# Optimization experiments

Measured on AMD Instinct MI355X. Metric: run time of the kernel, lower is better.

## Reference

```python
import jax, jax.numpy as jnp
import numpy as np

N, T, F = 4096, 24, 16          # nodes, seq_len, in_features
H = 128                          # temporal_hidden
NH, DO = 4, 32                   # gat num_heads, gat out_features (NH*DO == H)
SEM, PH = 64, 32                 # semantic hidden, predictor hidden
SLOPE = 0.2                      # leaky_relu negative slope
ADJ_P = 0.01                     # adjacency density


def setup_inputs() -> dict:
    key = jax.random.key(0)
    ks = jax.random.split(key, 40)
    f32 = jnp.float32

    def rn(k, shape, s=0.02):
        return jax.random.normal(k, shape, f32) * s

    features = jax.random.normal(ks[0], (N, T, F), f32)
    pos_adj = (jax.random.uniform(ks[1], (N, N)) < ADJ_P).astype(f32)
    neg_adj = (jax.random.uniform(ks[2], (N, N)) < ADJ_P).astype(f32)

    inp = dict(features=features, pos_adj=pos_adj, neg_adj=neg_adj)
    # GRU (torch layout: W_ih [3H,F], W_hh [3H,H], gate order r,z,n)
    inp['gru_Wih'] = rn(ks[3], (3 * H, F), 1.0 / np.sqrt(H))
    inp['gru_Whh'] = rn(ks[4], (3 * H, H), 1.0 / np.sqrt(H))
    inp['gru_bih'] = rn(ks[5], (3 * H,), 1.0 / np.sqrt(H))
    inp['gru_bhh'] = rn(ks[6], (3 * H,), 1.0 / np.sqrt(H))
    # GAT params (linear weights stored [in, out] so we use x @ W)
    i = 7
    for pre in ('pos', 'neg'):
        inp[pre + '_W'] = rn(ks[i], (H, NH * DO)); i += 1
        inp[pre + '_u'] = rn(ks[i], (NH, DO, 1), 1.0); i += 1
        inp[pre + '_v'] = rn(ks[i], (NH, DO, 1), 1.0); i += 1
        inp[pre + '_b'] = rn(ks[i], (1, NH * DO)); i += 1
        inp[pre + '_pW'] = rn(ks[i], (H, NH * DO)); i += 1
        inp[pre + '_pb'] = jnp.zeros((NH * DO,), f32)
    inp['self_W'] = rn(ks[i], (H, H)); i += 1
    inp['self_b'] = jnp.zeros((H,), f32)
    inp['mpos_W'] = rn(ks[i], (NH * DO, H)); i += 1
    inp['mpos_b'] = jnp.zeros((H,), f32)
    inp['mneg_W'] = rn(ks[i], (NH * DO, H)); i += 1
    inp['mneg_b'] = jnp.zeros((H,), f32)
    inp['sem_W1'] = rn(ks[i], (H, SEM)); i += 1
    inp['sem_b1'] = jnp.zeros((SEM,), f32)
    inp['sem_W2'] = rn(ks[i], (SEM, 1)); i += 1
    inp['pred_W1'] = rn(ks[i], (H, PH)); i += 1
    inp['pred_b1'] = jnp.zeros((PH,), f32)
    inp['pred_W2'] = rn(ks[i], (PH, 1)); i += 1
    inp['pred_b2'] = jnp.zeros((1,), f32)
    return inp


def _gru_last(x, Wih, Whh, bih, bhh):
    # x: [N, T, F] -> last hidden state [N, H]
    gi_all = jnp.einsum('ntf,gf->tng', x, Wih) + bih  # precompute input gates [T,N,3H]
    h0 = jnp.zeros((x.shape[0], Whh.shape[1]), x.dtype)

    def step(h, gi):
        gh = h @ Whh.T + bhh
        ir, iz, in_ = jnp.split(gi, 3, axis=-1)
        hr, hz, hn = jnp.split(gh, 3, axis=-1)
        r = jax.nn.sigmoid(ir + hr)
        z = jax.nn.sigmoid(iz + hz)
        n = jnp.tanh(in_ + r * hn)
        return (1.0 - z) * n + z * h, None

    h, _ = jax.lax.scan(step, h0, gi_all)
    return h


def _gat(x, adj, W, u, v, b, pW, pb):
    sup = (x @ W).reshape(-1, NH, DO).transpose(1, 0, 2)     # [NH, N, DO]
    f1 = jnp.matmul(sup, u).reshape(NH, 1, -1)               # [NH, 1, N]
    f2 = jnp.matmul(sup, v).reshape(NH, -1, 1)               # [NH, N, 1]
    w = jax.nn.leaky_relu(f1 + f2, SLOPE)                    # [NH, N, N]
    mw = w * adj                                             # mask
    rs = mw.sum(axis=2, keepdims=True)
    rs = jnp.where(rs == 0, jnp.ones_like(rs), rs)
    attn = mw / rs
    out = jnp.matmul(attn, sup).transpose(1, 0, 2).reshape(-1, NH * DO)
    return out + b + x @ pW + pb                             # bias + residual


def _pairnorm_si(x):
    x = x - x.mean(axis=0)
    rn = jnp.sqrt(1e-6 + (x * x).sum(axis=1, keepdims=True))
    return x / rn


def reference(features, pos_adj, neg_adj,
              gru_Wih, gru_Whh, gru_bih, gru_bhh,
              pos_W, pos_u, pos_v, pos_b, pos_pW, pos_pb,
              neg_W, neg_u, neg_v, neg_b, neg_pW, neg_pb,
              self_W, self_b, mpos_W, mpos_b, mneg_W, mneg_b,
              sem_W1, sem_b1, sem_W2,
              pred_W1, pred_b1, pred_W2, pred_b2):
    support = _gru_last(features, gru_Wih, gru_Whh, gru_bih, gru_bhh)  # [N, H]
    pos_sup = _gat(support, pos_adj, pos_W, pos_u, pos_v, pos_b, pos_pW, pos_pb)
    neg_sup = _gat(support, neg_adj, neg_W, neg_u, neg_v, neg_b, neg_pW, neg_pb)
    self_e = support @ self_W + self_b
    pos_e = pos_sup @ mpos_W + mpos_b
    neg_e = neg_sup @ mneg_W + mneg_b
    emb = jnp.stack([self_e, pos_e, neg_e], axis=1)          # [N, 3, H]
    w = jnp.tanh(emb @ sem_W1 + sem_b1) @ sem_W2             # [N, 3, 1]
    beta = jax.nn.softmax(w, axis=1)
    fused = (beta * emb).sum(axis=1)                          # [N, H]
    fused = _pairnorm_si(fused)
    h = jax.nn.relu(fused @ pred_W1 + pred_b1)               # dropout is eval no-op
    out = jax.nn.sigmoid(h @ pred_W2 + pred_b2).squeeze(-1)  # [N]
    return out
```

## Files before the change

### kernel.cpp

```cpp
#include <hip/hip_runtime.h>


#define NN 4096

typedef unsigned short u16;
typedef unsigned int   u32;
typedef unsigned long long u64;
typedef __attribute__((ext_vector_type(8))) short  short8;
typedef __attribute__((ext_vector_type(4))) float  float4v;

__device__ inline float bf2f(u16 u){ return __uint_as_float(((u32)u)<<16); }
__device__ inline u16 f2bf(float f){
  u32 x = __float_as_uint(f);
  return (u16)((x + 0x7fffu + ((x>>16)&1u))>>16);
}
__device__ inline float ldm(const void* p, int i, int bf){
  return bf ? bf2f(((const u16*)p)[i]) : ((const float*)p)[i];
}
__device__ inline u16 ldm16(const void* p, int i, int bf){
  return bf ? ((const u16*)p)[i] : f2bf(((const float*)p)[i]);
}
__device__ inline float fexp(float x){
  x = fminf(fmaxf(x,-80.f),80.f);
  return __builtin_amdgcn_exp2f(x*1.4426950408889634f);
}
__device__ inline float sigm_fast(float x){
  return __builtin_amdgcn_rcpf(1.f + __builtin_amdgcn_exp2f(-x*1.4426950408889634f));
}
__device__ inline float tanhf_(float x){
  float c = fminf(fmaxf(x,-15.f),15.f);
  float e = __builtin_amdgcn_exp2f(c*2.8853900817779268f);
  return (e-1.f)*__builtin_amdgcn_rcpf(e+1.f);
}
__device__ inline float4v mfma16(short8 a, short8 b, float4v c){
  return __builtin_amdgcn_mfma_f32_16x16x32_bf16(a,b,c,0,0,0);
}
__device__ inline int rdbf(const int* __restrict__ mflag){
  int b=0;
  #pragma unroll
  for (int k=0;k<16;k++) b|=mflag[k];
  return b;
}

__global__ __launch_bounds__(256) void k_detect(const u32* __restrict__ adj,
                                                int* __restrict__ mflag)
{
  __shared__ u32 w4[4];
  const int lane=threadIdx.x&63, wv=threadIdx.x>>6;
  int i = (blockIdx.x*256 + threadIdx.x)*4;
  uint4 v = *(const uint4*)(adj + i);
  u32 acc = (v.x | v.y | v.z | v.w) & 0xFFFFu;
  unsigned long long b = __ballot(acc != 0);
  if (lane==0) w4[wv] = (b!=0);
  __syncthreads();
  if (threadIdx.x==0) mflag[blockIdx.x] = (w4[0]|w4[1]|w4[2]|w4[3]) ? 1 : 0;
}

__global__ __launch_bounds__(256) void k_imp(
  const int* __restrict__ mflag,
  const void* gWih, const void* gWhh, const void* gbih, const void* gbhh,
  const void* posW, const void* posu, const void* posv, const void* posb,
  const void* pospW, const void* pospb,
  const void* negW, const void* negu, const void* negv, const void* negb,
  const void* negpW, const void* negpb,
  const void* selfW, const void* selfb, const void* mposW, const void* mposb,
  const void* mnegW, const void* mnegb,
  const void* semW1, const void* semb1, const void* semW2,
  const void* predW1, const void* predb1, const void* predW2, const void* predb2,
  u16* __restrict__ Wihb, u16* __restrict__ Whhb,
  u16* __restrict__ WT1,  u16* __restrict__ WT2,
  float* __restrict__ cbrz, float* __restrict__ cbin, float* __restrict__ cbhn,
  float* __restrict__ cuv,  float* __restrict__ cgb,  float* __restrict__ csb,
  float* __restrict__ cw1t, float* __restrict__ cb1,  float* __restrict__ cw2,
  float* __restrict__ cpw1t, float* __restrict__ cpb1, float* __restrict__ cpw2,
  float* __restrict__ cpb2, float* __restrict__ meanacc)
{
  const int bf = rdbf(mflag);
  int i = blockIdx.x*256 + threadIdx.x;
  if (i < 6144){ Wihb[i]=ldm16(gWih,i,bf); return; }  i-=6144;
  if (i < 49152){ Whhb[i]=ldm16(gWhh,i,bf); return; } i-=49152;
  if (i < 81920){
    int m=i>>7,k=i&127,sel=m>>7,ml=m&127;
    const void* s = sel==0?posW: sel==1?pospW: sel==2?negW: sel==3?negpW: selfW;
    WT1[i]=ldm16(s,k*128+ml,bf); return;
  } i-=81920;
  if (i < 32768){
    int m=i>>7,k=i&127;
    const void* s = (m<128)? mposW : mnegW;
    WT2[i]=ldm16(s,k*128+(m&127),bf); return;
  } i-=32768;
  if (i < 256){ cbrz[i]=ldm(gbih,i,bf)+ldm(gbhh,i,bf); return; } i-=256;
  if (i < 128){ cbin[i]=ldm(gbih,256+i,bf); return; } i-=128;
  if (i < 128){ cbhn[i]=ldm(gbhh,256+i,bf); return; } i-=128;
  if (i < 512){
    int s=i>>8, rem=i&255, wh=rem>>7, hd=rem&127;
    const void* p = s? (wh? negv:negu) : (wh? posv:posu);
    cuv[i]=ldm(p,hd,bf); return;
  } i-=512;
  if (i < 256){
    int s=i>>7, d=i&127;
    cgb[i]=ldm(s?negb:posb,d,bf)+ldm(s?negpb:pospb,d,bf); return;
  } i-=256;
  if (i < 384){
    int t=i>>7, d=i&127;
    const void* p = t==0? selfb : t==1? mposb : mnegb;
    csb[i]=ldm(p,d,bf); return;
  } i-=384;
  if (i < 8448){
    int c=i/132, k=i-c*132;
    cw1t[i] = (k<128)? ldm(semW1,k*64+c,bf) : 0.f; return;
  } i-=8448;
  if (i < 64){ cb1[i]=ldm(semb1,i,bf); return; } i-=64;
  if (i < 64){ cw2[i]=ldm(semW2,i,bf); return; } i-=64;
  if (i < 4224){
    int c=i/132, k=i-c*132;
    cpw1t[i] = (k<128)? ldm(predW1,k*32+c,bf) : 0.f; return;
  } i-=4224;
  if (i < 32){ cpb1[i]=ldm(predb1,i,bf); return; } i-=32;
  if (i < 32){ cpw2[i]=ldm(predW2,i,bf); return; } i-=32;
  if (i < 1){ cpb2[i]=ldm(predb2,i,bf); return; } i-=1;
  if (i < 128){ meanacc[i]=0.f; return; }
}

__global__ __launch_bounds__(512) void k_gruf(
  const int* __restrict__ mflag, const void* feat,
  const u16* __restrict__ Wihb, const u16* __restrict__ Whhb,
  const float* __restrict__ cbrz, const float* __restrict__ cbin,
  const float* __restrict__ cbhn,
  const u16* __restrict__ WT1, const float* __restrict__ cuv,
  const void* posadj, const void* negadj,
  u16* __restrict__ csri, int* __restrict__ csrc,
  u16* __restrict__ C1b, float* __restrict__ f12)
{
  __shared__ __attribute__((aligned(16))) u16 sh_x[16*392];
  __shared__ __attribute__((aligned(16))) u16 hbuf[2][16*136];
  const int bf = rdbf(mflag);
  const int tid=threadIdx.x, lane=tid&63, wv=tid>>6;

  if (blockIdx.x >= NN/16){
    const int c = blockIdx.x - NN/16;
    const int s = c >> 9;
    const int i = (c & 511)*8 + wv;
    const void* adj = s? negadj : posadj;
    u64 mask=0;
    if (bf){
      const u16* rp = (const u16*)adj + (size_t)i*4096;
      #pragma unroll
      for (int it=0; it<8; it++){
        const uint4 vv = *(const uint4*)(rp + it*512 + lane*8);
        u32 w[4]={vv.x,vv.y,vv.z,vv.w};
        #pragma unroll
        for (int q=0;q<4;q++){
          if (w[q]&0xffffu) mask |= 1ull<<(it*8+2*q);
          if (w[q]>>16)     mask |= 1ull<<(it*8+2*q+1);
        }
      }
    } else {
      const float* rp = (const float*)adj + (size_t)i*4096;
      #pragma unroll
      for (int it=0; it<16; it++){
        const uint4 vv = *(const uint4*)(rp + it*256 + lane*4);
        if (vv.x) mask |= 1ull<<(it*4+0);
        if (vv.y) mask |= 1ull<<(it*4+1);
        if (vv.z) mask |= 1ull<<(it*4+2);
        if (vv.w) mask |= 1ull<<(it*4+3);
      }
    }
    int cnt=__popcll(mask);
    int pre=cnt;
    #pragma unroll
    for (int off=1; off<64; off<<=1){
      int o=__shfl_up(pre,off);
      if (lane>=off) pre+=o;
    }
    const int base_p = pre-cnt;
    const int total  = __shfl(pre,63);
    u16* op = csri + ((size_t)s*4096 + i)*128;
    if (base_p < 128){
      u64 mm=mask; int p=base_p;
      while (mm && p<128){
        int b=__ffsll(mm)-1; mm&=mm-1;
        int e = bf ? ((b>>3)*512 + lane*8 + (b&7))
                   : ((b>>2)*256 + lane*4 + (b&3));
        op[p++]=(u16)e;
      }
    }
    if (lane==63) csrc[(size_t)s*4096 + i] = total>128 ? 128 : total;
    return;
  }

  const int quad=lane>>4, c15=lane&15;
  const int n0=blockIdx.x*16;

  if (bf){
    const u16* f16p=(const u16*)feat;
    for (int i=tid;i<768;i+=512){
      int n=i/48, c=(i-n*48)*8;
      *(uint4*)(sh_x + n*392 + c) =
        *(const uint4*)(f16p + (size_t)(n0+n)*384 + c);
    }
  } else {
    const float* f32p=(const float*)feat;
    for (int i=tid;i<1536;i+=512){
      int n=i/96, c=(i-n*96)*4;
      float4 v = *(const float4*)(f32p + (size_t)(n0+n)*384 + c);
      uint2 pk;
      pk.x = (u32)f2bf(v.x) | ((u32)f2bf(v.y)<<16);
      pk.y = (u32)f2bf(v.z) | ((u32)f2bf(v.w)<<16);
      *(uint2*)(sh_x + n*392 + c) = pk;
    }
  }
  for (int i=tid;i<16*136;i+=512) hbuf[0][i]=0;

  const short8 z8={0,0,0,0,0,0,0,0};
  const float4v z4={0.f,0.f,0.f,0.f};
  short8 bh[3][4], bx3[3];
  #pragma unroll
  for (int g=0;g<3;g++){
    int rowb=(g*8+wv)*16+c15;
    #pragma unroll
    for (int ks=0;ks<4;ks++) bh[g][ks]=*(const short8*)(Whhb+(size_t)rowb*128+ks*32+quad*8);
    bx3[g] = (quad<2)? *(const short8*)(Wihb+(size_t)rowb*16+quad*8) : z8;
  }
  const int j0=wv*16+c15;
  const float brz_r=cbrz[j0], brz_z=cbrz[128+j0];
  const float bin0=cbin[j0],  bhn0=cbhn[j0];
  float hr[4]={0.f,0.f,0.f,0.f};
  __syncthreads();

  for (int t=0;t<24;t++){
    const u16* hb  = hbuf[t&1];
    u16*       hbn = hbuf[(t+1)&1];
    short8 ah[4];
    #pragma unroll
    for (int ks=0;ks<4;ks++) ah[ks]=*(const short8*)(hb + c15*136 + ks*32 + quad*8);
    short8 ax = (quad<2)? *(const short8*)(sh_x + c15*392 + t*16 + quad*8) : z8;
    float4v racc = mfma16(ax,bx3[0],z4);
    float4v zacc = mfma16(ax,bx3[1],z4);
    float4v ni   = mfma16(ax,bx3[2],z4);
    float4v nh   = z4;
    #pragma unroll
    for (int ks=0;ks<4;ks++){
      racc = mfma16(ah[ks],bh[0][ks],racc);
      zacc = mfma16(ah[ks],bh[1][ks],zacc);
      nh   = mfma16(ah[ks],bh[2][ks],nh);
    }
    #pragma unroll
    for (int rr=0;rr<4;rr++){
      const int node = quad*4+rr;
      float r_ = sigm_fast(racc[rr]+brz_r);
      float z_ = sigm_fast(zacc[rr]+brz_z);
      float n_ = tanhf_(ni[rr]+bin0 + r_*(nh[rr]+bhn0));
      float hv = (1.f-z_)*n_ + z_*hr[rr];
      hr[rr]=hv; hbn[node*136+j0]=f2bf(hv);
    }
    __syncthreads();
  }
  short8 a[4];
  #pragma unroll
  for (int ks=0;ks<4;ks++) a[ks]=*(const short8*)(hbuf[0]+c15*136+ks*32+quad*8);
  #pragma unroll
  for (int q=0;q<5;q++){
    int tile=wv*5+q;
    float4v acc={0.f,0.f,0.f,0.f};
    #pragma unroll
    for (int ks=0;ks<4;ks++){
      short8 b=*(const short8*)(WT1+(size_t)(tile*16+c15)*128+ks*32+quad*8);
      acc=mfma16(a[ks],b,acc);
    }
    #pragma unroll
    for (int r=0;r<4;r++)
      C1b[(size_t)(n0+quad*4+r)*640 + tile*16 + c15]=f2bf(acc[r]);
  }
  __syncthreads();
  {
    int q=tid;
    int nl=q&15, h=(q>>4)&3, wsel=(q>>6)&1, s=(q>>7)&1;
    const float* uvp = cuv + s*256 + wsel*128 + h*32;
    const u16*   SL  = C1b + (size_t)(n0+nl)*640 + s*256 + h*32;
    float t=0.f;
    #pragma unroll
    for (int d=0;d<32;d++) t += bf2f(SL[d])*uvp[d];
    f12[s*32768 + wsel*16384 + h*4096 + (n0+nl)] = t;
  }
}

__global__ __launch_bounds__(1024) void k_gat3(
  const u16* __restrict__ csri, const int* __restrict__ csrc,
  const u16* __restrict__ C1b, const float* __restrict__ f12,
  const float* __restrict__ cgb, const u16* __restrict__ WT2,
  float* __restrict__ E)
{
  __shared__ u16   nbuf[16][128];
  __shared__ float wbuf[16][4][128];
  __shared__ __attribute__((aligned(16))) u16 sA[16*136];
  const int s=blockIdx.y;
  const int wv=threadIdx.x>>6, lane=threadIdx.x&63;
  const int n0=blockIdx.x*16;
  const int i=n0+wv;

  ((u32*)nbuf[wv])[lane] = ((const u32*)(csri + ((size_t)s*4096 + i)*128))[lane];
  const int dg = csrc[(size_t)s*4096 + i];

  const float* f1 = f12 + s*32768;
  const float* f2 = f12 + s*32768 + 16384;
  const int d0=lane, d1=lane+64, h0=lane>>5, h1=2+(lane>>5);
  float f2v[4];
  #pragma unroll
  for (int h=0;h<4;h++) f2v[h]=f2[h*4096+i];
  for (int e=lane; e<dg; e+=64){
    int j = nbuf[wv][e];
    #pragma unroll
    for (int h=0;h<4;h++){
      float w = f1[h*4096+j] + f2v[h];
      wbuf[wv][h][e] = w>0.f ? w : 0.2f*w;
    }
  }

  float acc0=0.f,acc1=0.f,rs0=0.f,rs1=0.f;
  #pragma unroll 4
  for (int e=0;e<dg;e++){
    float w0 = wbuf[wv][h0][e];
    float w1 = wbuf[wv][h1][e];
    int j = nbuf[wv][e];
    const u16* SL = C1b + (size_t)j*640 + s*256;
    acc0 += w0*bf2f(SL[d0]); rs0 += w0;
    acc1 += w1*bf2f(SL[d1]); rs1 += w1;
  }
  if (rs0==0.f) rs0=1.f;
  if (rs1==0.f) rs1=1.f;
  const u16* P = C1b + (size_t)i*640 + s*256 + 128;
  sA[wv*136+d0]=f2bf(acc0/rs0 + cgb[s*128+d0] + bf2f(P[d0]));
  sA[wv*136+d1]=f2bf(acc1/rs1 + cgb[s*128+d1] + bf2f(P[d1]));
  __syncthreads();
  if (wv<8){
    const int quad=lane>>4, c15=lane&15;
    short8 a[4];
    #pragma unroll
    for (int ks=0;ks<4;ks++) a[ks]=*(const short8*)(sA+c15*136+ks*32+quad*8);
    const int tile=wv;
    float4v acc={0.f,0.f,0.f,0.f};
    #pragma unroll
    for (int ks=0;ks<4;ks++){
      short8 b=*(const short8*)(WT2+(size_t)(s*128+tile*16+c15)*128+ks*32+quad*8);
      acc=mfma16(a[ks],b,acc);
    }
    #pragma unroll
    for (int r=0;r<4;r++) E[(size_t)(n0+quad*4+r)*256 + s*128 + tile*16 + c15]=acc[r];
  }
}

__global__ __launch_bounds__(256) void k_sem(
  const u16* __restrict__ C1b, const float* __restrict__ E,
  const float* __restrict__ csb, const float* __restrict__ cw1t,
  const float* __restrict__ cb1, const float* __restrict__ cw2,
  float* __restrict__ fused, float* __restrict__ meanacc)
{
  __shared__ float sW1t[64*132];
  __shared__ float sW2[64];
  __shared__ float sb1[64];
  __shared__ float sE[4][3][128];
  __shared__ float redm[4][128];
  const int tid=threadIdx.x, wv=tid>>6, lane=tid&63;
  for (int i=tid;i<8448;i+=256) sW1t[i]=cw1t[i];
  if (tid<64){ sW2[tid]=cw2[tid]; sb1[tid]=cb1[tid]; }
  __syncthreads();
  const float* wcol = sW1t + lane*132;
  float macc0=0.f, macc1=0.f;
  for (int u=0;u<4;u++){
    const int n = blockIdx.x*16 + wv*4 + u;
    for (int d=lane; d<128; d+=64){
      sE[wv][0][d] = bf2f(C1b[(size_t)n*640+512+d]) + csb[d];
      sE[wv][1][d] = E[(size_t)n*256 + d]    + csb[128+d];
      sE[wv][2][d] = E[(size_t)n*256+128+d]  + csb[256+d];
    }
    float sc[3];
    #pragma unroll
    for (int s=0;s<3;s++){
      float t = sb1[lane];
      #pragma unroll
      for (int k=0;k<128;k+=4){
        float4 e4 = *(const float4*)&sE[wv][s][k];
        float4 w4 = *(const float4*)&wcol[k];
        t += e4.x*w4.x + e4.y*w4.y + e4.z*w4.z + e4.w*w4.w;
      }
      t = tanhf_(t);
      float p = t*sW2[lane];
      #pragma unroll
      for (int off=32; off; off>>=1) p += __shfl_xor(p, off);
      sc[s]=p;
    }
    float mx = fmaxf(sc[0], fmaxf(sc[1],sc[2]));
    float e0=fexp(sc[0]-mx), e1=fexp(sc[1]-mx), e2=fexp(sc[2]-mx);
    float inv = 1.f/(e0+e1+e2);
    float b0=e0*inv, b1=e1*inv, b2=e2*inv;
    float f0 = b0*sE[wv][0][lane]    + b1*sE[wv][1][lane]    + b2*sE[wv][2][lane];
    float f1 = b0*sE[wv][0][lane+64] + b1*sE[wv][1][lane+64] + b2*sE[wv][2][lane+64];
    fused[(size_t)n*128+lane]    = f0;
    fused[(size_t)n*128+64+lane] = f1;
    macc0 += f0; macc1 += f1;
  }
  redm[wv][lane]=macc0; redm[wv][lane+64]=macc1;
  __syncthreads();
  if (tid<128)
    atomicAdd(&meanacc[tid], redm[0][tid]+redm[1][tid]+redm[2][tid]+redm[3][tid]);
}

__global__ __launch_bounds__(256) void k_pred(
  const float* __restrict__ fused, const float* __restrict__ meanacc,
  const float* __restrict__ cpw1t, const float* __restrict__ cpb1,
  const float* __restrict__ cpw2, const float* __restrict__ cpb2,
  float* __restrict__ out)
{
  __shared__ float sy[4][128];
  __shared__ float sW1t[32*132];
  __shared__ float sW2[32];
  const int tid=threadIdx.x, wv=tid>>6, lane=tid&63;
  for (int i=tid;i<4224;i+=256) sW1t[i]=cpw1t[i];
  if (tid<32) sW2[tid]=cpw2[tid];
  const int n = blockIdx.x*4 + wv;
  const float inv_n = 1.f/4096.f;
  float x0 = fused[(size_t)n*128+lane]    - meanacc[lane]*inv_n;
  float x1 = fused[(size_t)n*128+64+lane] - meanacc[64+lane]*inv_n;
  float ss = x0*x0 + x1*x1;
  #pragma unroll
  for (int o=32;o;o>>=1) ss += __shfl_xor(ss,o);
  float ir = 1.f/sqrtf(1e-6f + ss);
  sy[wv][lane]=x0*ir; sy[wv][64+lane]=x1*ir;
  __syncthreads();
  const int c = lane&31, half = lane>>5;
  const float* wcol = sW1t + c*132 + half*64;
  const float* yrow = sy[wv] + half*64;
  float h=0.f;
  #pragma unroll
  for (int k=0;k<64;k+=4){
    float4 y4 = *(const float4*)&yrow[k];
    float4 w4 = *(const float4*)&wcol[k];
    h += y4.x*w4.x + y4.y*w4.y + y4.z*w4.z + y4.w*w4.w;
  }
  h += __shfl_xor(h,32);
  h += cpb1[c];
  h = h>0.f? h : 0.f;
  float p = h*sW2[c];
  #pragma unroll
  for (int o=16;o;o>>=1) p += __shfl_xor(p,o);
  if (!lane){
    float z = p + cpb2[0];
    out[n] = __builtin_amdgcn_rcpf(1.f + fexp(-z));
  }
}

extern "C" void kernel_launch(void* const* d_in, const int* in_sizes, int n_in,
                              void* d_out, int out_size, void* d_ws, size_t ws_size,
                              hipStream_t stream)
{
  const void* feat  =d_in[0];
  const void* posadj=d_in[1];
  const void* negadj=d_in[2];
  const void* gWih  =d_in[3];
  const void* gWhh  =d_in[4];
  const void* gbih  =d_in[5];
  const void* gbhh  =d_in[6];
  const void* posW  =d_in[7];
  const void* posu  =d_in[8];
  const void* posv  =d_in[9];
  const void* posb  =d_in[10];
  const void* pospW =d_in[11];
  const void* pospb =d_in[12];
  const void* negW  =d_in[13];
  const void* negu  =d_in[14];
  const void* negv  =d_in[15];
  const void* negb  =d_in[16];
  const void* negpW =d_in[17];
  const void* negpb =d_in[18];
  const void* selfW =d_in[19];
  const void* selfb =d_in[20];
  const void* mposW =d_in[21];
  const void* mposb =d_in[22];
  const void* mnegW =d_in[23];
  const void* mnegb =d_in[24];
  const void* semW1 =d_in[25];
  const void* semb1 =d_in[26];
  const void* semW2 =d_in[27];
  const void* predW1=d_in[28];
  const void* predb1=d_in[29];
  const void* predW2=d_in[30];
  const void* predb2=d_in[31];

  char* wsb=(char*)d_ws; size_t off=0;
  auto alloc=[&](size_t bytes)->void*{ void* p=wsb+off; off+=(bytes+255)&~(size_t)255; return p; };
  int*   mflag=(int*)  alloc(256);
  u16*   Wihb =(u16*)  alloc(6144*2);
  u16*   Whhb =(u16*)  alloc(49152*2);
  u16*   WT1  =(u16*)  alloc(81920*2);
  u16*   WT2  =(u16*)  alloc(32768*2);
  float* cbrz =(float*)alloc(256*4);
  float* cbin =(float*)alloc(128*4);
  float* cbhn =(float*)alloc(128*4);
  float* cuv  =(float*)alloc(512*4);
  float* cgb  =(float*)alloc(256*4);
  float* csb  =(float*)alloc(384*4);
  float* cw1t =(float*)alloc(8448*4);
  float* cb1  =(float*)alloc(64*4);
  float* cw2  =(float*)alloc(64*4);
  float* cpw1t=(float*)alloc(4224*4);
  float* cpb1 =(float*)alloc(32*4);
  float* cpw2 =(float*)alloc(32*4);
  float* cpb2 =(float*)alloc(4);
  u16*   C1b  =(u16*)  alloc((size_t)NN*640*2);
  float* f12  =(float*)alloc((size_t)65536*4);
  float* E    =(float*)alloc((size_t)NN*256*4);
  float* fused=(float*)alloc((size_t)NN*128*4);
  float* meanacc=(float*)alloc(128*4);
  u16*   csri =(u16*)  alloc((size_t)2*4096*128*2);
  int*   csrc =(int*)  alloc((size_t)2*4096*4);
  (void)ws_size; (void)in_sizes; (void)n_in; (void)out_size;

  k_detect<<<16,          256,0,stream>>>((const u32*)posadj,mflag);
  k_imp   <<<722,         256,0,stream>>>(mflag,gWih,gWhh,gbih,gbhh,
              posW,posu,posv,posb,pospW,pospb,negW,negu,negv,negb,negpW,negpb,
              selfW,selfb,mposW,mposb,mnegW,mnegb,semW1,semb1,semW2,
              predW1,predb1,predW2,predb2,
              Wihb,Whhb,WT1,WT2,cbrz,cbin,cbhn,cuv,cgb,csb,cw1t,cb1,cw2,
              cpw1t,cpb1,cpw2,cpb2,meanacc);
  k_gruf  <<<NN/16+1024,  512,0,stream>>>(mflag,feat,Wihb,Whhb,cbrz,cbin,cbhn,
                                          WT1,cuv,posadj,negadj,csri,csrc,
                                          C1b,f12);
  k_gat3  <<<dim3(256,2),1024,0,stream>>>(csri,csrc,C1b,f12,cgb,WT2,E);
  k_sem   <<<NN/16,       256,0,stream>>>(C1b,E,csb,cw1t,cb1,cw2,fused,meanacc);
  k_pred  <<<NN/4,        256,0,stream>>>(fused,meanacc,cpw1t,cpb1,cpw2,cpb2,(float*)d_out);
}
```

Measured before the change: 269.3 us.

## Split neg-adjacency CSR build between GRU kernel and GAT kernel

Only the first NEG_CSR rows of the negative adjacency are compacted into CSR inside the GRU kernel. The GAT kernel now builds neighbor lists for the remaining negative rows on the fly from the dense adjacency. The aim is to shrink the adjacency-scan tail of the GRU launch by moving part of that scan into the GAT kernel. The cost is that GAT blocks for those rows must read a full dense row each, which adds latency and makes blocks unbalanced.

```diff
diff --git a/kernel.cpp b/kernel.cpp
--- a/kernel.cpp
+++ b/kernel.cpp
@@ -2,6 +2,7 @@
 
 
 #define NN 4096
+#define NEG_CSR 1024
 
 typedef unsigned short u16;
 typedef unsigned int   u32;
@@ -138,9 +139,9 @@
   const int tid=threadIdx.x, lane=tid&63, wv=tid>>6;
 
   if (blockIdx.x >= NN/16){
-    const int c = blockIdx.x - NN/16;
-    const int s = c >> 9;
-    const int i = (c & 511)*8 + wv;
+    const int t = (blockIdx.x - NN/16)*8 + wv;
+    const int s = (t >= 4096) ? 1 : 0;
+    const int i = s ? (t - 4096) : t;
     const void* adj = s? negadj : posadj;
     u64 mask=0;
     if (bf){
@@ -286,6 +287,8 @@
 }
 
 __global__ __launch_bounds__(1024) void k_gat3(
+  const int* __restrict__ mflag,
+  const void* posadj, const void* negadj,
   const u16* __restrict__ csri, const int* __restrict__ csrc,
   const u16* __restrict__ C1b, const float* __restrict__ f12,
   const float* __restrict__ cgb, const u16* __restrict__ WT2,
@@ -299,8 +302,56 @@
   const int n0=blockIdx.x*16;
   const int i=n0+wv;
 
-  ((u32*)nbuf[wv])[lane] = ((const u32*)(csri + ((size_t)s*4096 + i)*128))[lane];
-  const int dg = csrc[(size_t)s*4096 + i];
+  int dg;
+  if (s==1 && n0 >= NEG_CSR){
+    const int bf = rdbf(mflag);
+    u64 mask=0;
+    if (bf){
+      const u16* rp = (const u16*)negadj + (size_t)i*4096;
+      #pragma unroll
+      for (int it=0; it<8; it++){
+        const uint4 vv = *(const uint4*)(rp + it*512 + lane*8);
+        u32 w[4]={vv.x,vv.y,vv.z,vv.w};
+        #pragma unroll
+        for (int q=0;q<4;q++){
+          if (w[q]&0xffffu) mask |= 1ull<<(it*8+2*q);
+          if (w[q]>>16)     mask |= 1ull<<(it*8+2*q+1);
+        }
+      }
+    } else {
+      const float* rp = (const float*)negadj + (size_t)i*4096;
+      #pragma unroll
+      for (int it=0; it<16; it++){
+        const uint4 vv = *(const uint4*)(rp + it*256 + lane*4);
+        if (vv.x) mask |= 1ull<<(it*4+0);
+        if (vv.y) mask |= 1ull<<(it*4+1);
+        if (vv.z) mask |= 1ull<<(it*4+2);
+        if (vv.w) mask |= 1ull<<(it*4+3);
+      }
+    }
+    int cnt=__popcll(mask);
+    int pre=cnt;
+    #pragma unroll
+    for (int off=1; off<64; off<<=1){
+      int o=__shfl_up(pre,off);
+      if (lane>=off) pre+=o;
+    }
+    const int base_p = pre-cnt;
+    const int total  = __shfl(pre,63);
+    if (base_p < 128){
+      u64 mm=mask; int p=base_p;
+      while (mm && p<128){
+        int b=__ffsll(mm)-1; mm&=mm-1;
+        int e = bf ? ((b>>3)*512 + lane*8 + (b&7))
+                   : ((b>>2)*256 + lane*4 + (b&3));
+        nbuf[wv][p++]=(u16)e;
+      }
+    }
+    dg = total>128 ? 128 : total;
+  } else {
+    ((u32*)nbuf[wv])[lane] = ((const u32*)(csri + ((size_t)s*4096 + i)*128))[lane];
+    dg = csrc[(size_t)s*4096 + i];
+  }
 
   const float* f1 = f12 + s*32768;
   const float* f2 = f12 + s*32768 + 16384;
@@ -523,10 +574,11 @@
               predW1,predb1,predW2,predb2,
               Wihb,Whhb,WT1,WT2,cbrz,cbin,cbhn,cuv,cgb,csb,cw1t,cb1,cw2,
               cpw1t,cpb1,cpw2,cpb2,meanacc);
-  k_gruf  <<<NN/16+1024,  512,0,stream>>>(mflag,feat,Wihb,Whhb,cbrz,cbin,cbhn,
-                                          WT1,cuv,posadj,negadj,csri,csrc,
-                                          C1b,f12);
-  k_gat3  <<<dim3(256,2),1024,0,stream>>>(csri,csrc,C1b,f12,cgb,WT2,E);
+  k_gruf  <<<NN/16 + (NN+NEG_CSR)/8, 512,0,stream>>>(mflag,feat,Wihb,Whhb,
+                                          cbrz,cbin,cbhn,WT1,cuv,
+                                          posadj,negadj,csri,csrc,C1b,f12);
+  k_gat3  <<<dim3(256,2),1024,0,stream>>>(mflag,posadj,negadj,csri,csrc,
+                                          C1b,f12,cgb,WT2,E);
   k_sem   <<<NN/16,       256,0,stream>>>(C1b,E,csb,cw1t,cb1,cw2,fused,meanacc);
   k_pred  <<<NN/4,        256,0,stream>>>(fused,meanacc,cpw1t,cpb1,cpw2,cpb2,(float*)d_out);
 }
```

Result: no change. 271.2 us, median of 2 (+0.7%).

## Fold dtype detection and weight preprocessing into consumer kernels

Applied to the files above, without the earlier changes.

Removes the separate detect and weight-conversion kernels. Every consumer kernel now detects per block whether the inputs are bf16 by sampling the adjacency matrix, then loads and converts the original weights directly, including transposed strided reads for the MFMA B operands. This saves two kernel launches and the intermediate buffers they filled. In exchange each block repeats a small detection read and barrier, and the transposed weight loads become strided and uncoalesced.

```diff
diff --git a/kernel.cpp b/kernel.cpp
--- a/kernel.cpp
+++ b/kernel.cpp
@@ -35,112 +35,63 @@
 __device__ inline float4v mfma16(short8 a, short8 b, float4v c){
   return __builtin_amdgcn_mfma_f32_16x16x32_bf16(a,b,c,0,0,0);
 }
-__device__ inline int rdbf(const int* __restrict__ mflag){
-  int b=0;
-  #pragma unroll
-  for (int k=0;k<16;k++) b|=mflag[k];
-  return b;
-}
-
-__global__ __launch_bounds__(256) void k_detect(const u32* __restrict__ adj,
-                                                int* __restrict__ mflag)
-{
-  __shared__ u32 w4[4];
-  const int lane=threadIdx.x&63, wv=threadIdx.x>>6;
-  int i = (blockIdx.x*256 + threadIdx.x)*4;
-  uint4 v = *(const uint4*)(adj + i);
-  u32 acc = (v.x | v.y | v.z | v.w) & 0xFFFFu;
-  unsigned long long b = __ballot(acc != 0);
-  if (lane==0) w4[wv] = (b!=0);
-  __syncthreads();
-  if (threadIdx.x==0) mflag[blockIdx.x] = (w4[0]|w4[1]|w4[2]|w4[3]) ? 1 : 0;
-}
-
-__global__ __launch_bounds__(256) void k_imp(
-  const int* __restrict__ mflag,
+
+__device__ inline int detect_bf_blk(const u32* __restrict__ adj, int tid,
+                                    int* __restrict__ sflag){
+  if (tid==0) *sflag=0;
+  __syncthreads();
+  u32 nz=0;
+  if (tid<256){
+    #pragma unroll
+    for (int q=0;q<4;q++){
+      const uint4 v = *(const uint4*)(adj + tid*4 + q*4096);
+      nz |= (v.x|v.y|v.z|v.w);
+    }
+  }
+  const u64 b = __ballot((nz&0xFFFFu)!=0);
+  if ((tid&63)==0 && b) atomicOr(sflag,1);
+  __syncthreads();
+  return *sflag;
+}
+
+__device__ inline short8 ld8w(const void* p, size_t idx, int bf){
+  if (bf) return *(const short8*)((const u16*)p + idx);
+  const float* f=(const float*)p+idx;
+  const float4 a=*(const float4*)f, b=*(const float4*)(f+4);
+  short8 r;
+  r[0]=(short)f2bf(a.x); r[1]=(short)f2bf(a.y); r[2]=(short)f2bf(a.z); r[3]=(short)f2bf(a.w);
+  r[4]=(short)f2bf(b.x); r[5]=(short)f2bf(b.y); r[6]=(short)f2bf(b.z); r[7]=(short)f2bf(b.w);
+  return r;
+}
+__device__ inline short8 ld8wT(const void* p, int k, int m, int bf){
+  short8 r;
+  #pragma unroll
+  for (int j=0;j<8;j++) r[j]=(short)ldm16(p,(k+j)*128+m,bf);
+  return r;
+}
+
+__global__ __launch_bounds__(512) void k_gruf(
+  const void* feat,
   const void* gWih, const void* gWhh, const void* gbih, const void* gbhh,
-  const void* posW, const void* posu, const void* posv, const void* posb,
-  const void* pospW, const void* pospb,
-  const void* negW, const void* negu, const void* negv, const void* negb,
-  const void* negpW, const void* negpb,
-  const void* selfW, const void* selfb, const void* mposW, const void* mposb,
-  const void* mnegW, const void* mnegb,
-  const void* semW1, const void* semb1, const void* semW2,
-  const void* predW1, const void* predb1, const void* predW2, const void* predb2,
-  u16* __restrict__ Wihb, u16* __restrict__ Whhb,
-  u16* __restrict__ WT1,  u16* __restrict__ WT2,
-  float* __restrict__ cbrz, float* __restrict__ cbin, float* __restrict__ cbhn,
-  float* __restrict__ cuv,  float* __restrict__ cgb,  float* __restrict__ csb,
-  float* __restrict__ cw1t, float* __restrict__ cb1,  float* __restrict__ cw2,
-  float* __restrict__ cpw1t, float* __restrict__ cpb1, float* __restrict__ cpw2,
-  float* __restrict__ cpb2, float* __restrict__ meanacc)
-{
-  const int bf = rdbf(mflag);
-  int i = blockIdx.x*256 + threadIdx.x;
-  if (i < 6144){ Wihb[i]=ldm16(gWih,i,bf); return; }  i-=6144;
-  if (i < 49152){ Whhb[i]=ldm16(gWhh,i,bf); return; } i-=49152;
-  if (i < 81920){
-    int m=i>>7,k=i&127,sel=m>>7,ml=m&127;
-    const void* s = sel==0?posW: sel==1?pospW: sel==2?negW: sel==3?negpW: selfW;
-    WT1[i]=ldm16(s,k*128+ml,bf); return;
-  } i-=81920;
-  if (i < 32768){
-    int m=i>>7,k=i&127;
-    const void* s = (m<128)? mposW : mnegW;
-    WT2[i]=ldm16(s,k*128+(m&127),bf); return;
-  } i-=32768;
-  if (i < 256){ cbrz[i]=ldm(gbih,i,bf)+ldm(gbhh,i,bf); return; } i-=256;
-  if (i < 128){ cbin[i]=ldm(gbih,256+i,bf); return; } i-=128;
-  if (i < 128){ cbhn[i]=ldm(gbhh,256+i,bf); return; } i-=128;
-  if (i < 512){
-    int s=i>>8, rem=i&255, wh=rem>>7, hd=rem&127;
-    const void* p = s? (wh? negv:negu) : (wh? posv:posu);
-    cuv[i]=ldm(p,hd,bf); return;
-  } i-=512;
-  if (i < 256){
-    int s=i>>7, d=i&127;
-    cgb[i]=ldm(s?negb:posb,d,bf)+ldm(s?negpb:pospb,d,bf); return;
-  } i-=256;
-  if (i < 384){
-    int t=i>>7, d=i&127;
-    const void* p = t==0? selfb : t==1? mposb : mnegb;
-    csb[i]=ldm(p,d,bf); return;
-  } i-=384;
-  if (i < 8448){
-    int c=i/132, k=i-c*132;
-    cw1t[i] = (k<128)? ldm(semW1,k*64+c,bf) : 0.f; return;
-  } i-=8448;
-  if (i < 64){ cb1[i]=ldm(semb1,i,bf); return; } i-=64;
-  if (i < 64){ cw2[i]=ldm(semW2,i,bf); return; } i-=64;
-  if (i < 4224){
-    int c=i/132, k=i-c*132;
-    cpw1t[i] = (k<128)? ldm(predW1,k*32+c,bf) : 0.f; return;
-  } i-=4224;
-  if (i < 32){ cpb1[i]=ldm(predb1,i,bf); return; } i-=32;
-  if (i < 32){ cpw2[i]=ldm(predW2,i,bf); return; } i-=32;
-  if (i < 1){ cpb2[i]=ldm(predb2,i,bf); return; } i-=1;
-  if (i < 128){ meanacc[i]=0.f; return; }
-}
-
-__global__ __launch_bounds__(512) void k_gruf(
-  const int* __restrict__ mflag, const void* feat,
-  const u16* __restrict__ Wihb, const u16* __restrict__ Whhb,
-  const float* __restrict__ cbrz, const float* __restrict__ cbin,
-  const float* __restrict__ cbhn,
-  const u16* __restrict__ WT1, const float* __restrict__ cuv,
+  const void* posW, const void* pospW, const void* negW, const void* negpW,
+  const void* selfW,
+  const void* posu, const void* posv, const void* negu, const void* negv,
   const void* posadj, const void* negadj,
   u16* __restrict__ csri, int* __restrict__ csrc,
-  u16* __restrict__ C1b, float* __restrict__ f12)
+  u16* __restrict__ C1b, float* __restrict__ f12,
+  float* __restrict__ meanacc)
 {
   __shared__ __attribute__((aligned(16))) u16 sh_x[16*392];
   __shared__ __attribute__((aligned(16))) u16 hbuf[2][16*136];
-  const int bf = rdbf(mflag);
+  __shared__ int s_bf;
   const int tid=threadIdx.x, lane=tid&63, wv=tid>>6;
+  const int bf = detect_bf_blk((const u32*)posadj, tid, &s_bf);
+  if (blockIdx.x==0 && tid<128) meanacc[tid]=0.f;
 
   if (blockIdx.x >= NN/16){
-    const int c = blockIdx.x - NN/16;
-    const int s = c >> 9;
-    const int i = (c & 511)*8 + wv;
+    const int t = (blockIdx.x - NN/16)*8 + wv;
+    const int s = t >> 12;
+    const int i = t & 4095;
     const void* adj = s? negadj : posadj;
     u64 mask=0;
     if (bf){
@@ -219,12 +170,13 @@
   for (int g=0;g<3;g++){
     int rowb=(g*8+wv)*16+c15;
     #pragma unroll
-    for (int ks=0;ks<4;ks++) bh[g][ks]=*(const short8*)(Whhb+(size_t)rowb*128+ks*32+quad*8);
-    bx3[g] = (quad<2)? *(const short8*)(Wihb+(size_t)rowb*16+quad*8) : z8;
+    for (int ks=0;ks<4;ks++) bh[g][ks]=ld8w(gWhh,(size_t)rowb*128+ks*32+quad*8,bf);
+    bx3[g] = (quad<2)? ld8w(gWih,(size_t)rowb*16+quad*8,bf) : z8;
   }
   const int j0=wv*16+c15;
-  const float brz_r=cbrz[j0], brz_z=cbrz[128+j0];
-  const float bin0=cbin[j0],  bhn0=cbhn[j0];
+  const float brz_r=ldm(gbih,j0,bf)+ldm(gbhh,j0,bf);
+  const float brz_z=ldm(gbih,128+j0,bf)+ldm(gbhh,128+j0,bf);
+  const float bin0=ldm(gbih,256+j0,bf), bhn0=ldm(gbhh,256+j0,bf);
   float hr[4]={0.f,0.f,0.f,0.f};
   __syncthreads();
 
@@ -261,13 +213,13 @@
   for (int ks=0;ks<4;ks++) a[ks]=*(const short8*)(hbuf[0]+c15*136+ks*32+quad*8);
   #pragma unroll
   for (int q=0;q<5;q++){
-    int tile=wv*5+q;
+    const int tile=wv*5+q;
+    const int row=tile*16+c15, sel=row>>7, ml=row&127;
+    const void* Ws = sel==0?posW: sel==1?pospW: sel==2?negW: sel==3?negpW: selfW;
     float4v acc={0.f,0.f,0.f,0.f};
     #pragma unroll
-    for (int ks=0;ks<4;ks++){
-      short8 b=*(const short8*)(WT1+(size_t)(tile*16+c15)*128+ks*32+quad*8);
-      acc=mfma16(a[ks],b,acc);
-    }
+    for (int ks=0;ks<4;ks++)
+      acc=mfma16(a[ks], ld8wT(Ws, ks*32+quad*8, ml, bf), acc);
     #pragma unroll
     for (int r=0;r<4;r++)
       C1b[(size_t)(n0+quad*4+r)*640 + tile*16 + c15]=f2bf(acc[r]);
@@ -276,26 +228,31 @@
   {
     int q=tid;
     int nl=q&15, h=(q>>4)&3, wsel=(q>>6)&1, s=(q>>7)&1;
-    const float* uvp = cuv + s*256 + wsel*128 + h*32;
-    const u16*   SL  = C1b + (size_t)(n0+nl)*640 + s*256 + h*32;
+    const void* uvp = s? (wsel? negv:negu) : (wsel? posv:posu);
+    const u16*  SL  = C1b + (size_t)(n0+nl)*640 + s*256 + h*32;
     float t=0.f;
     #pragma unroll
-    for (int d=0;d<32;d++) t += bf2f(SL[d])*uvp[d];
+    for (int d=0;d<32;d++) t += bf2f(SL[d])*ldm(uvp,h*32+d,bf);
     f12[s*32768 + wsel*16384 + h*4096 + (n0+nl)] = t;
   }
 }
 
 __global__ __launch_bounds__(1024) void k_gat3(
+  const void* posadj,
   const u16* __restrict__ csri, const int* __restrict__ csrc,
   const u16* __restrict__ C1b, const float* __restrict__ f12,
-  const float* __restrict__ cgb, const u16* __restrict__ WT2,
+  const void* posb, const void* pospb, const void* negb, const void* negpb,
+  const void* mposW, const void* mnegW,
   float* __restrict__ E)
 {
   __shared__ u16   nbuf[16][128];
   __shared__ float wbuf[16][4][128];
   __shared__ __attribute__((aligned(16))) u16 sA[16*136];
+  __shared__ int s_bf;
+  const int tid=threadIdx.x;
+  const int bf = detect_bf_blk((const u32*)posadj, tid, &s_bf);
   const int s=blockIdx.y;
-  const int wv=threadIdx.x>>6, lane=threadIdx.x&63;
+  const int wv=tid>>6, lane=tid&63;
   const int n0=blockIdx.x*16;
   const int i=n0+wv;
 
@@ -329,9 +286,11 @@
   }
   if (rs0==0.f) rs0=1.f;
   if (rs1==0.f) rs1=1.f;
+  const float cg0 = ldm(s?negb:posb,d0,bf)+ldm(s?negpb:pospb,d0,bf);
+  const float cg1 = ldm(s?negb:posb,d1,bf)+ldm(s?negpb:pospb,d1,bf);
   const u16* P = C1b + (size_t)i*640 + s*256 + 128;
-  sA[wv*136+d0]=f2bf(acc0/rs0 + cgb[s*128+d0] + bf2f(P[d0]));
-  sA[wv*136+d1]=f2bf(acc1/rs1 + cgb[s*128+d1] + bf2f(P[d1]));
+  sA[wv*136+d0]=f2bf(acc0/rs0 + cg0 + bf2f(P[d0]));
+  sA[wv*136+d1]=f2bf(acc1/rs1 + cg1 + bf2f(P[d1]));
   __syncthreads();
   if (wv<8){
     const int quad=lane>>4, c15=lane&15;
@@ -339,21 +298,21 @@
     #pragma unroll
     for (int ks=0;ks<4;ks++) a[ks]=*(const short8*)(sA+c15*136+ks*32+quad*8);
     const int tile=wv;
+    const void* mW = s? mnegW : mposW;
     float4v acc={0.f,0.f,0.f,0.f};
     #pragma unroll
-    for (int ks=0;ks<4;ks++){
-      short8 b=*(const short8*)(WT2+(size_t)(s*128+tile*16+c15)*128+ks*32+quad*8);
-      acc=mfma16(a[ks],b,acc);
-    }
+    for (int ks=0;ks<4;ks++)
+      acc=mfma16(a[ks], ld8wT(mW, ks*32+quad*8, tile*16+c15, bf), acc);
     #pragma unroll
     for (int r=0;r<4;r++) E[(size_t)(n0+quad*4+r)*256 + s*128 + tile*16 + c15]=acc[r];
   }
 }
 
 __global__ __launch_bounds__(256) void k_sem(
+  const void* posadj,
   const u16* __restrict__ C1b, const float* __restrict__ E,
-  const float* __restrict__ csb, const float* __restrict__ cw1t,
-  const float* __restrict__ cb1, const float* __restrict__ cw2,
+  const void* selfb, const void* mposb, const void* mnegb,
+  const void* semW1, const void* semb1, const void* semW2,
   float* __restrict__ fused, float* __restrict__ meanacc)
 {
   __shared__ float sW1t[64*132];
@@ -361,19 +320,28 @@
   __shared__ float sb1[64];
   __shared__ float sE[4][3][128];
   __shared__ float redm[4][128];
+  __shared__ int s_bf;
   const int tid=threadIdx.x, wv=tid>>6, lane=tid&63;
-  for (int i=tid;i<8448;i+=256) sW1t[i]=cw1t[i];
-  if (tid<64){ sW2[tid]=cw2[tid]; sb1[tid]=cb1[tid]; }
-  __syncthreads();
+  const int bf = detect_bf_blk((const u32*)posadj, tid, &s_bf);
+  for (int i=tid;i<8448;i+=256){
+    int c=i/132, k=i-c*132;
+    sW1t[i] = (k<128)? ldm(semW1,k*64+c,bf) : 0.f;
+  }
+  if (tid<64){ sW2[tid]=ldm(semW2,tid,bf); sb1[tid]=ldm(semb1,tid,bf); }
+  __syncthreads();
+  const float cs0a=ldm(selfb,lane,bf), cs0b=ldm(selfb,lane+64,bf);
+  const float cs1a=ldm(mposb,lane,bf), cs1b=ldm(mposb,lane+64,bf);
+  const float cs2a=ldm(mnegb,lane,bf), cs2b=ldm(mnegb,lane+64,bf);
   const float* wcol = sW1t + lane*132;
   float macc0=0.f, macc1=0.f;
   for (int u=0;u<4;u++){
     const int n = blockIdx.x*16 + wv*4 + u;
-    for (int d=lane; d<128; d+=64){
-      sE[wv][0][d] = bf2f(C1b[(size_t)n*640+512+d]) + csb[d];
-      sE[wv][1][d] = E[(size_t)n*256 + d]    + csb[128+d];
-      sE[wv][2][d] = E[(size_t)n*256+128+d]  + csb[256+d];
-    }
+    sE[wv][0][lane]    = bf2f(C1b[(size_t)n*640+512+lane])    + cs0a;
+    sE[wv][0][lane+64] = bf2f(C1b[(size_t)n*640+512+lane+64]) + cs0b;
+    sE[wv][1][lane]    = E[(size_t)n*256 + lane]        + cs1a;
+    sE[wv][1][lane+64] = E[(size_t)n*256 + lane+64]     + cs1b;
+    sE[wv][2][lane]    = E[(size_t)n*256+128+lane]      + cs2a;
+    sE[wv][2][lane+64] = E[(size_t)n*256+128+lane+64]   + cs2b;
     float sc[3];
     #pragma unroll
     for (int s=0;s<3;s++){
@@ -407,17 +375,22 @@
 }
 
 __global__ __launch_bounds__(256) void k_pred(
+  const void* posadj,
   const float* __restrict__ fused, const float* __restrict__ meanacc,
-  const float* __restrict__ cpw1t, const float* __restrict__ cpb1,
-  const float* __restrict__ cpw2, const float* __restrict__ cpb2,
+  const void* predW1, const void* predb1, const void* predW2, const void* predb2,
   float* __restrict__ out)
 {
   __shared__ float sy[4][128];
   __shared__ float sW1t[32*132];
   __shared__ float sW2[32];
+  __shared__ int s_bf;
   const int tid=threadIdx.x, wv=tid>>6, lane=tid&63;
-  for (int i=tid;i<4224;i+=256) sW1t[i]=cpw1t[i];
-  if (tid<32) sW2[tid]=cpw2[tid];
+  const int bf = detect_bf_blk((const u32*)posadj, tid, &s_bf);
+  for (int i=tid;i<4224;i+=256){
+    int c=i/132, k=i-c*132;
+    sW1t[i] = (k<128)? ldm(predW1,k*32+c,bf) : 0.f;
+  }
+  if (tid<32) sW2[tid]=ldm(predW2,tid,bf);
   const int n = blockIdx.x*4 + wv;
   const float inv_n = 1.f/4096.f;
   float x0 = fused[(size_t)n*128+lane]    - meanacc[lane]*inv_n;
@@ -439,13 +412,13 @@
     h += y4.x*w4.x + y4.y*w4.y + y4.z*w4.z + y4.w*w4.w;
   }
   h += __shfl_xor(h,32);
-  h += cpb1[c];
+  h += ldm(predb1,c,bf);
   h = h>0.f? h : 0.f;
   float p = h*sW2[c];
   #pragma unroll
   for (int o=16;o;o>>=1) p += __shfl_xor(p,o);
   if (!lane){
-    float z = p + cpb2[0];
+    float z = p + ldm(predb2,0,bf);
     out[n] = __builtin_amdgcn_rcpf(1.f + fexp(-z));
   }
 }
@@ -489,24 +462,6 @@
 
   char* wsb=(char*)d_ws; size_t off=0;
   auto alloc=[&](size_t bytes)->void*{ void* p=wsb+off; off+=(bytes+255)&~(size_t)255; return p; };
-  int*   mflag=(int*)  alloc(256);
-  u16*   Wihb =(u16*)  alloc(6144*2);
-  u16*   Whhb =(u16*)  alloc(49152*2);
-  u16*   WT1  =(u16*)  alloc(81920*2);
-  u16*   WT2  =(u16*)  alloc(32768*2);
-  float* cbrz =(float*)alloc(256*4);
-  float* cbin =(float*)alloc(128*4);
-  float* cbhn =(float*)alloc(128*4);
-  float* cuv  =(float*)alloc(512*4);
-  float* cgb  =(float*)alloc(256*4);
-  float* csb  =(float*)alloc(384*4);
-  float* cw1t =(float*)alloc(8448*4);
-  float* cb1  =(float*)alloc(64*4);
-  float* cw2  =(float*)alloc(64*4);
-  float* cpw1t=(float*)alloc(4224*4);
-  float* cpb1 =(float*)alloc(32*4);
-  float* cpw2 =(float*)alloc(32*4);
-  float* cpb2 =(float*)alloc(4);
   u16*   C1b  =(u16*)  alloc((size_t)NN*640*2);
   float* f12  =(float*)alloc((size_t)65536*4);
   float* E    =(float*)alloc((size_t)NN*256*4);
@@ -516,17 +471,14 @@
   int*   csrc =(int*)  alloc((size_t)2*4096*4);
   (void)ws_size; (void)in_sizes; (void)n_in; (void)out_size;
 
-  k_detect<<<16,          256,0,stream>>>((const u32*)posadj,mflag);
-  k_imp   <<<722,         256,0,stream>>>(mflag,gWih,gWhh,gbih,gbhh,
-              posW,posu,posv,posb,pospW,pospb,negW,negu,negv,negb,negpW,negpb,
-              selfW,selfb,mposW,mposb,mnegW,mnegb,semW1,semb1,semW2,
-              predW1,predb1,predW2,predb2,
-              Wihb,Whhb,WT1,WT2,cbrz,cbin,cbhn,cuv,cgb,csb,cw1t,cb1,cw2,
-              cpw1t,cpb1,cpw2,cpb2,meanacc);
-  k_gruf  <<<NN/16+1024,  512,0,stream>>>(mflag,feat,Wihb,Whhb,cbrz,cbin,cbhn,
-                                          WT1,cuv,posadj,negadj,csri,csrc,
-                                          C1b,f12);
-  k_gat3  <<<dim3(256,2),1024,0,stream>>>(csri,csrc,C1b,f12,cgb,WT2,E);
-  k_sem   <<<NN/16,       256,0,stream>>>(C1b,E,csb,cw1t,cb1,cw2,fused,meanacc);
-  k_pred  <<<NN/4,        256,0,stream>>>(fused,meanacc,cpw1t,cpb1,cpw2,cpb2,(float*)d_out);
-}
+  k_gruf  <<<NN/16+1024, 512,0,stream>>>(feat,gWih,gWhh,gbih,gbhh,
+                                         posW,pospW,negW,negpW,selfW,
+                                         posu,posv,negu,negv,
+                                         posadj,negadj,csri,csrc,C1b,f12,meanacc);
+  k_gat3  <<<dim3(256,2),1024,0,stream>>>(posadj,csri,csrc,C1b,f12,
+                                          posb,pospb,negb,negpb,mposW,mnegW,E);
+  k_sem   <<<NN/16,      256,0,stream>>>(posadj,C1b,E,selfb,mposb,mnegb,
+                                         semW1,semb1,semW2,fused,meanacc);
+  k_pred  <<<NN/4,       256,0,stream>>>(posadj,fused,meanacc,
+                                         predW1,predb1,predW2,predb2,(float*)d_out);
+}
```

New measurement: 342.3 us. 27.1% more time.
